# Kernel optimization log

Measured on AMD Instinct MI355X. Metric: run time of the kernel, lower is better.

## Reference

```python
import jax, jax.numpy as jnp
import numpy as np

DIM, HEADS = 1024, 16
HEAD_DIM = DIM // HEADS
SCALE = HEAD_DIM ** -0.5


def setup_inputs() -> dict:
    key = jax.random.key(0)
    ks = jax.random.split(key, 5)
    B, N = 2, 2048
    x = jax.random.normal(ks[0], (B, N, DIM), dtype=jnp.float32)
    freqs = jax.random.normal(ks[1], (N, HEAD_DIM // 2), dtype=jnp.float32)
    w_qkv = jax.random.normal(ks[2], (3 * DIM, DIM), dtype=jnp.float32) * 0.02
    w_proj = jax.random.normal(ks[3], (DIM, DIM), dtype=jnp.float32) * 0.02
    b_proj = jnp.zeros((DIM,), dtype=jnp.float32)
    return {"x": x, "freqs": freqs, "w_qkv": w_qkv, "w_proj": w_proj, "b_proj": b_proj}


def _apply_rotary(t, cos, sin):
    # t: (B,N,H,D); cos/sin: (1,N,1,D//2)
    B, N, H, D = t.shape
    tp = t.reshape(B, N, H, D // 2, 2)
    x1, x2 = tp[..., 0], tp[..., 1]
    out = jnp.stack([x1 * cos - x2 * sin, x1 * sin + x2 * cos], axis=-1)
    return out.reshape(B, N, H, D)


def reference(x, freqs, w_qkv, w_proj, b_proj):
    B, N, C = x.shape
    H, D = HEADS, HEAD_DIM
    qkv = (x @ w_qkv.T).reshape(B, N, 3, H, D)  # fused QKV projection
    q, k, v = qkv[:, :, 0], qkv[:, :, 1], qkv[:, :, 2]  # each (B,N,H,D)
    cos = jnp.cos(freqs)[None, :, None, :]  # (1,N,1,D/2)
    sin = jnp.sin(freqs)[None, :, None, :]
    q = _apply_rotary(q, cos, sin)
    k = _apply_rotary(k, cos, sin)
    # SDPA: scores (B,H,N,N)
    scores = jnp.einsum("bqhd,bkhd->bhqk", q, k) * SCALE
    attn = jax.nn.softmax(scores, axis=-1)
    out = jnp.einsum("bhqk,bkhd->bqhd", attn, v).reshape(B, N, C)
    return out @ w_proj.T + b_proj
```

## Files before the change

### kernel.cpp

```cpp
#include <hip/hip_runtime.h>
#include <hip/hip_bf16.h>
#include <stdint.h>

#define BATCH   2
#define SEQ     2048
#define CDIM    1024
#define NHEAD   16
#define HDIM    64
#define MROWS   (BATCH*SEQ)
#define QKVN    (3*CDIM)
#define QSCALE  0.18033688011112042f

typedef __hip_bfloat16 bf16;
using bf16x8 = __attribute__((ext_vector_type(8))) __bf16;
using f32x4  = __attribute__((ext_vector_type(4))) float;
using s16x4  = __attribute__((ext_vector_type(4))) short;

__device__ __forceinline__ void gld16(const void* g, void* l) {
    __builtin_amdgcn_global_load_lds(
        (__attribute__((address_space(1))) void*)(void*)(g),
        (__attribute__((address_space(3))) void*)(l),
        16, 0, 0);
}

__device__ __forceinline__ f32x4 mfma16x16x32(bf16x8 a, bf16x8 b, f32x4 c) {
    return __builtin_amdgcn_mfma_f32_16x16x32_bf16(a, b, c, 0, 0, 0);
}
__device__ __forceinline__ f32x4 mfma16x16x16(s16x4 a, s16x4 b, f32x4 c) {
    return __builtin_amdgcn_mfma_f32_16x16x16bf16_1k(a, b, c, 0, 0, 0);
}

__device__ __forceinline__ uint16_t bfbits(float v) {
    bf16 b = __float2bfloat16(v);
    return *(uint16_t*)&b;
}
__device__ __forceinline__ uint32_t pkbf(float a, float b) {
    uint32_t au = __builtin_bit_cast(uint32_t, a);
    uint32_t bu = __builtin_bit_cast(uint32_t, b);
    return ((au + 0x8000u) >> 16) | ((bu + 0x8000u) & 0xffff0000u);
}

#define NX_F4 ((size_t)MROWS*CDIM/4)
#define NQ_F4 ((size_t)QKVN*CDIM/4)
#define NP_F4 ((size_t)CDIM*CDIM/4)
#define NF_SC ((size_t)SEQ*32)

__global__ __launch_bounds__(256)
void cvt_kernel(const float* __restrict__ x, const float* __restrict__ wq,
                const float* __restrict__ wp, const float* __restrict__ freqs,
                bf16* __restrict__ xb, bf16* __restrict__ wqb,
                bf16* __restrict__ wpb, float2* __restrict__ csn) {
    size_t i4 = (size_t)blockIdx.x*256 + threadIdx.x;
    if (i4 < NX_F4 + NQ_F4 + NP_F4) {
        const float* src; bf16* dst; size_t off;
        if (i4 < NX_F4)           { src = x;  dst = xb;  off = i4; }
        else if (i4 < NX_F4+NQ_F4){ src = wq; dst = wqb; off = i4 - NX_F4; }
        else                      { src = wp; dst = wpb; off = i4 - NX_F4 - NQ_F4; }
        float4 v = ((const float4*)src)[off];
        bf16 o[4] = { __float2bfloat16(v.x), __float2bfloat16(v.y),
                      __float2bfloat16(v.z), __float2bfloat16(v.w) };
        *(uint64_t*)(dst + off*4) = *(const uint64_t*)o;
    } else if (i4 < NX_F4 + NQ_F4 + NP_F4 + NF_SC) {
        size_t k = i4 - (NX_F4 + NQ_F4 + NP_F4);
        float f = freqs[k];
        csn[k] = make_float2(cosf(f), sinf(f));
    }
}

__global__ __launch_bounds__(256)
void gemm_qkv_rope(const bf16* __restrict__ A, const bf16* __restrict__ Bw,
                   const float2* __restrict__ csn, bf16* __restrict__ Qr,
                   bf16* __restrict__ Kr, bf16* __restrict__ VG) {
    const int K = CDIM;
    __shared__ __align__(16) bf16 sh[64*136];
    bf16* As = sh;
    bf16* Bs = sh + 4096;

    const int bm = blockIdx.x, bn = blockIdx.y;
    const int tid  = threadIdx.x;
    const int lane = tid & 63;
    const int w    = tid >> 6;
    const int wm   = (w & 1) * 64;
    const int wn   = (w >> 1) * 64;
    const int quad = lane >> 4;
    const int l16  = lane & 15;

    const int c0 = tid, c1 = tid + 256;
    const size_t a_off0 = (size_t)(bm*128 + (c0 >> 2)) * K + (c0 & 3) * 8;
    const size_t a_off1 = (size_t)(bm*128 + (c1 >> 2)) * K + (c1 & 3) * 8;
    const size_t b_off0 = (size_t)(bn*128 + (c0 >> 2)) * K + (c0 & 3) * 8;
    const size_t b_off1 = (size_t)(bn*128 + (c1 >> 2)) * K + (c1 & 3) * 8;

    f32x4 acc[4][4] = {};

    for (int k0 = 0; k0 < K; k0 += 32) {
        __syncthreads();
        gld16(A + a_off0 + k0, &As[c0*8]);
        gld16(A + a_off1 + k0, &As[c1*8]);
        gld16(Bw + b_off0 + k0, &Bs[c0*8]);
        gld16(Bw + b_off1 + k0, &Bs[c1*8]);
        __syncthreads();

        bf16x8 af[4], bfv[4];
#pragma unroll
        for (int i = 0; i < 4; i++)
            af[i] = *(const bf16x8*)&As[(wm + i*16 + l16)*32 + quad*8];
#pragma unroll
        for (int i = 0; i < 4; i++)
            bfv[i] = *(const bf16x8*)&Bs[(wn + i*16 + l16)*32 + quad*8];
#pragma unroll
        for (int mi = 0; mi < 4; mi++)
#pragma unroll
            for (int ni = 0; ni < 4; ni++)
                acc[mi][ni] = mfma16x16x32(af[mi], bfv[ni], acc[mi][ni]);
    }

    const int region = bn >> 3;
    if (region < 2) {
        bf16* dst = region ? Kr : Qr;
        const float qs = region ? 1.0f : QSCALE;
        const int odd = l16 & 1;
#pragma unroll
        for (int mi = 0; mi < 4; mi++) {
#pragma unroll
            for (int ni = 0; ni < 4; ni++) {
                const int cq = (bn & 7)*128 + wn + ni*16 + l16;
                const int h = cq >> 6, d = cq & 63, fi = d >> 1;
#pragma unroll
                for (int r = 0; r < 4; r++) {
                    const int m = bm*128 + wm + mi*16 + quad*4 + r;
                    const int bb = m >> 11, n = m & 2047;
                    float own = acc[mi][ni][r];
                    float prt = __shfl_xor(own, 1);
                    float2 cs2 = csn[n*32 + fi];
                    float o = odd ? (prt*cs2.y + own*cs2.x)
                                  : (own*cs2.x - prt*cs2.y);
                    dst[((size_t)(bb*16 + h)*SEQ + n)*HDIM + d] =
                        __float2bfloat16(o * qs);
                }
            }
        }
    } else {
        const int bb = (bm*128) >> 11, n0l = (bm*128) & 2047;
        __syncthreads();
#pragma unroll
        for (int cc = 0; cc < 2; ++cc) {
            if ((w >> 1) == cc) {
#pragma unroll
                for (int mi = 0; mi < 4; mi++)
#pragma unroll
                    for (int ni = 0; ni < 4; ni++) {
                        const int d  = ni*16 + l16;
                        const int tl = wm + mi*16 + quad*4;
                        uint2 pk;
                        pk.x = (uint32_t)bfbits(acc[mi][ni][0]) |
                               ((uint32_t)bfbits(acc[mi][ni][1]) << 16);
                        pk.y = (uint32_t)bfbits(acc[mi][ni][2]) |
                               ((uint32_t)bfbits(acc[mi][ni][3]) << 16);
                        *(uint2*)&sh[d*136 + tl] = pk;
                    }
            }
            __syncthreads();
            const int h = (bn - 16)*2 + cc;
            bf16* vg = VG + (size_t)(bb*16 + h) * (SEQ*HDIM);
#pragma unroll
            for (int k = 0; k < 8; k++) {
                int s8   = tid + 256*k;
                int tile = s8 >> 10, si = s8 & 1023;
                int g  = si >> 6,  ln = si & 63;
                int j  = g >> 2,   dt = g & 3;
                int qk = ln >> 4,  ld = ln & 15;
                int tl = tile*64 + j*16 + qk*4;
                int d  = dt*16 + ld;
                *(uint2*)&vg[(size_t)((n0l >> 6) + tile)*4096 + si*4] =
                    *(const uint2*)&sh[d*136 + tl];
            }
            __syncthreads();
        }
    }
}

__global__ __launch_bounds__(256)
void gemm_proj(const bf16* __restrict__ A, const bf16* __restrict__ Bw,
               const float* __restrict__ bias, float* __restrict__ C,
               int M, int N, int K) {
    __shared__ __align__(16) bf16 As[64*32];
    __shared__ __align__(16) bf16 Bs[128*32];

    const int bm = blockIdx.x, bn = blockIdx.y;
    const int tid  = threadIdx.x;
    const int lane = tid & 63;
    const int w    = tid >> 6;
    const int wm   = (w & 1) * 32;
    const int wn   = (w >> 1) * 64;
    const int quad = lane >> 4;
    const int l16  = lane & 15;

    const int ca = tid, cb0 = tid, cb1 = tid + 256;
    const size_t a_off  = (size_t)(bm*64  + (ca  >> 2)) * K + (ca  & 3) * 8;
    const size_t b_off0 = (size_t)(bn*128 + (cb0 >> 2)) * K + (cb0 & 3) * 8;
    const size_t b_off1 = (size_t)(bn*128 + (cb1 >> 2)) * K + (cb1 & 3) * 8;

    f32x4 acc[2][4] = {};

    for (int k0 = 0; k0 < K; k0 += 32) {
        __syncthreads();
        gld16(A + a_off + k0, &As[ca*8]);
        gld16(Bw + b_off0 + k0, &Bs[cb0*8]);
        gld16(Bw + b_off1 + k0, &Bs[cb1*8]);
        __syncthreads();

        bf16x8 af[2], bfv[4];
#pragma unroll
        for (int i = 0; i < 2; i++)
            af[i] = *(const bf16x8*)&As[(wm + i*16 + l16)*32 + quad*8];
#pragma unroll
        for (int i = 0; i < 4; i++)
            bfv[i] = *(const bf16x8*)&Bs[(wn + i*16 + l16)*32 + quad*8];
#pragma unroll
        for (int mi = 0; mi < 2; mi++)
#pragma unroll
            for (int ni = 0; ni < 4; ni++)
                acc[mi][ni] = mfma16x16x32(af[mi], bfv[ni], acc[mi][ni]);
    }

#pragma unroll
    for (int mi = 0; mi < 2; mi++) {
        const int r0 = bm*64 + wm + mi*16 + quad*4;
#pragma unroll
        for (int ni = 0; ni < 4; ni++) {
            const int c = bn*128 + wn + ni*16 + l16;
            const float bv = bias[c];
#pragma unroll
            for (int r = 0; r < 4; r++)
                C[(size_t)(r0 + r)*N + c] = acc[mi][ni][r] + bv;
        }
    }
}

__global__ __launch_bounds__(64)
void attn_kernel(const bf16* __restrict__ Qr, const bf16* __restrict__ Kr,
                 const bf16* __restrict__ VG, bf16* __restrict__ Ao) {
    const int blk = blockIdx.x;
    const int bh  = blk >> 5;
    const int b   = bh >> 4, h = bh & 15;
    const int q0  = (blk & 31) * 64;
    const int lane = threadIdx.x;
    const int quad = lane >> 4, l16 = lane & 15;

    bf16x8 qf[4][2];
#pragma unroll
    for (int t = 0; t < 4; t++) {
        const int qrow = q0 + t*16 + l16;
        const bf16* qp = Qr + ((size_t)bh*SEQ + qrow)*HDIM + quad*8;
        qf[t][0] = *(const bf16x8*)(qp);
        qf[t][1] = *(const bf16x8*)(qp + 32);
    }

    const bf16* KrB = Kr + (size_t)bh*SEQ*HDIM;
    const bf16* VgB = VG + (size_t)bh*SEQ*HDIM;

    f32x4 acc[4][4] = {};
    float lsum[4] = {};

    bf16x8 kb0[4][2], kb1[4][2];

#pragma unroll
    for (int j = 0; j < 4; j++) {
        const bf16* kr = KrB + (size_t)(j*16 + l16)*HDIM + quad*8;
        kb0[j][0] = *(const bf16x8*)(kr);
        kb0[j][1] = *(const bf16x8*)(kr + 32);
    }

    auto step = [&](bf16x8 (&kc)[4][2], bf16x8 (&kn)[4][2], int it) {
        s16x4 vfr[16];
        const bf16* vt = VgB + (size_t)it*4096;
#pragma unroll
        for (int m = 0; m < 16; m++)
            vfr[m] = *(const s16x4*)&vt[(m*64 + lane)*4];

        if (it + 1 < SEQ/64) {
            const bf16* kr = KrB + (size_t)((it+1)*64 + l16)*HDIM + quad*8;
#pragma unroll
            for (int j = 0; j < 4; j++) {
                kn[j][0] = *(const bf16x8*)(kr + j*16*HDIM);
                kn[j][1] = *(const bf16x8*)(kr + j*16*HDIM + 32);
            }
        }

#pragma unroll
        for (int j = 0; j < 4; j++) {
            s16x4 pf[4];
#pragma unroll
            for (int t = 0; t < 4; t++) {
                f32x4 sv = {};
                sv = mfma16x16x32(kc[j][0], qf[t][0], sv);
                sv = mfma16x16x32(kc[j][1], qf[t][1], sv);
                float e0 = __builtin_amdgcn_exp2f(sv[0]);
                float e1 = __builtin_amdgcn_exp2f(sv[1]);
                float e2 = __builtin_amdgcn_exp2f(sv[2]);
                float e3 = __builtin_amdgcn_exp2f(sv[3]);
                lsum[t] += (e0 + e1) + (e2 + e3);
                union { uint32_t u[2]; s16x4 v; } pa;
                pa.u[0] = pkbf(e0, e1);
                pa.u[1] = pkbf(e2, e3);
                pf[t] = pa.v;
            }
#pragma unroll
            for (int dt = 0; dt < 4; dt++) {
                s16x4 vf = vfr[j*4 + dt];
#pragma unroll
                for (int t = 0; t < 4; t++)
                    acc[t][dt] = mfma16x16x16(pf[t], vf, acc[t][dt]);
            }
        }
    };

    for (int it2 = 0; it2 < SEQ/128; ++it2) {
        step(kb0, kb1, it2*2);
        step(kb1, kb0, it2*2 + 1);
    }

#pragma unroll
    for (int t = 0; t < 4; t++) {
        lsum[t] += __shfl_xor(lsum[t], 16, 64);
        lsum[t] += __shfl_xor(lsum[t], 32, 64);
    }
    float lt[4][4];
#pragma unroll
    for (int t = 0; t < 4; t++)
#pragma unroll
        for (int r = 0; r < 4; r++)
            lt[t][r] = __shfl(lsum[t], quad*20 + r, 64);

#pragma unroll
    for (int t = 0; t < 4; t++)
#pragma unroll
        for (int dt = 0; dt < 4; dt++)
#pragma unroll
            for (int r = 0; r < 4; r++) {
                int qr  = q0 + t*16 + quad*4 + r;
                int col = h*HDIM + dt*16 + l16;
                Ao[(size_t)(b*SEQ + qr)*CDIM + col] =
                    __float2bfloat16(acc[t][dt][r] / lt[t][r]);
            }
}

extern "C" void kernel_launch(void* const* d_in, const int* in_sizes, int n_in,
                              void* d_out, int out_size, void* d_ws, size_t ws_size,
                              hipStream_t stream) {
    const float* x      = (const float*)d_in[0];
    const float* freqs  = (const float*)d_in[1];
    const float* w_qkv  = (const float*)d_in[2];
    const float* w_proj = (const float*)d_in[3];
    const float* b_proj = (const float*)d_in[4];
    float* out = (float*)d_out;

    char* ws = (char*)d_ws;
    bf16*   xb    = (bf16*)ws;   ws += (size_t)MROWS * CDIM * sizeof(bf16);
    bf16*   wqkvb = (bf16*)ws;   ws += (size_t)QKVN * CDIM * sizeof(bf16);
    bf16*   wprojb= (bf16*)ws;   ws += (size_t)CDIM * CDIM * sizeof(bf16);
    float2* csn   = (float2*)ws; ws += (size_t)SEQ * 32 * sizeof(float2);
    bf16*   Qr    = (bf16*)ws;   ws += (size_t)BATCH*NHEAD*SEQ*HDIM*sizeof(bf16);
    bf16*   Kr    = (bf16*)ws;   ws += (size_t)BATCH*NHEAD*SEQ*HDIM*sizeof(bf16);
    bf16*   VG    = (bf16*)ws;   ws += (size_t)BATCH*NHEAD*SEQ*HDIM*sizeof(bf16);
    bf16*   Ao    = (bf16*)ws;

    {
        size_t nthr = NX_F4 + NQ_F4 + NP_F4 + NF_SC;
        cvt_kernel<<<dim3((nthr + 255) / 256), dim3(256), 0, stream>>>(
            x, w_qkv, w_proj, freqs, xb, wqkvb, wprojb, csn);
    }
    gemm_qkv_rope<<<dim3(MROWS/128, QKVN/128), dim3(256), 0, stream>>>(
        xb, wqkvb, csn, Qr, Kr, VG);
    attn_kernel<<<dim3(BATCH*NHEAD*(SEQ/64)), dim3(64), 0, stream>>>(
        Qr, Kr, VG, Ao);
    gemm_proj<<<dim3(MROWS/64, CDIM/128), dim3(256), 0, stream>>>(
        Ao, wprojb, b_proj, out, MROWS, CDIM, CDIM);
}
```

Before: 229.2 us.

## Stage attention K/V through double-buffered LDS and write V directly from QKV epilogue

```diff
diff --git a/kernel.cpp b/kernel.cpp
--- a/kernel.cpp
+++ b/kernel.cpp
@@ -72,9 +72,8 @@
                    const float2* __restrict__ csn, bf16* __restrict__ Qr,
                    bf16* __restrict__ Kr, bf16* __restrict__ VG) {
     const int K = CDIM;
-    __shared__ __align__(16) bf16 sh[64*136];
-    bf16* As = sh;
-    bf16* Bs = sh + 4096;
+    __shared__ __align__(16) bf16 As[128*32];
+    __shared__ __align__(16) bf16 Bs[128*32];
 
     const int bm = blockIdx.x, bn = blockIdx.y;
     const int tid  = threadIdx.x;
@@ -141,41 +140,23 @@
             }
         }
     } else {
-        const int bb = (bm*128) >> 11, n0l = (bm*128) & 2047;
-        __syncthreads();
-#pragma unroll
-        for (int cc = 0; cc < 2; ++cc) {
-            if ((w >> 1) == cc) {
-#pragma unroll
-                for (int mi = 0; mi < 4; mi++)
-#pragma unroll
-                    for (int ni = 0; ni < 4; ni++) {
-                        const int d  = ni*16 + l16;
-                        const int tl = wm + mi*16 + quad*4;
-                        uint2 pk;
-                        pk.x = (uint32_t)bfbits(acc[mi][ni][0]) |
-                               ((uint32_t)bfbits(acc[mi][ni][1]) << 16);
-                        pk.y = (uint32_t)bfbits(acc[mi][ni][2]) |
-                               ((uint32_t)bfbits(acc[mi][ni][3]) << 16);
-                        *(uint2*)&sh[d*136 + tl] = pk;
-                    }
-            }
-            __syncthreads();
-            const int h = (bn - 16)*2 + cc;
-            bf16* vg = VG + (size_t)(bb*16 + h) * (SEQ*HDIM);
-#pragma unroll
-            for (int k = 0; k < 8; k++) {
-                int s8   = tid + 256*k;
-                int tile = s8 >> 10, si = s8 & 1023;
-                int g  = si >> 6,  ln = si & 63;
-                int j  = g >> 2,   dt = g & 3;
-                int qk = ln >> 4,  ld = ln & 15;
-                int tl = tile*64 + j*16 + qk*4;
-                int d  = dt*16 + ld;
-                *(uint2*)&vg[(size_t)((n0l >> 6) + tile)*4096 + si*4] =
-                    *(const uint2*)&sh[d*136 + tl];
-            }
-            __syncthreads();
+        const int bb  = (bm*128) >> 11, n0l = (bm*128) & 2047;
+        const int h   = (bn - 16)*2 + (wn >> 6);
+        bf16* vg = VG + (size_t)(bb*16 + h) * (SEQ*HDIM);
+#pragma unroll
+        for (int mi = 0; mi < 4; mi++) {
+            const int tile = (n0l >> 6) + ((wm + mi*16) >> 6);
+            const int j    = ((wm + mi*16) >> 4) & 3;
+#pragma unroll
+            for (int ni = 0; ni < 4; ni++) {
+                uint2 pk;
+                pk.x = (uint32_t)bfbits(acc[mi][ni][0]) |
+                       ((uint32_t)bfbits(acc[mi][ni][1]) << 16);
+                pk.y = (uint32_t)bfbits(acc[mi][ni][2]) |
+                       ((uint32_t)bfbits(acc[mi][ni][3]) << 16);
+                const int slot = (j*4 + ni)*64 + quad*16 + l16;
+                *(uint2*)&vg[(size_t)tile*4096 + slot*4] = pk;
+            }
         }
     }
 }
@@ -247,6 +228,10 @@
     const int q0  = (blk & 31) * 64;
     const int lane = threadIdx.x;
     const int quad = lane >> 4, l16 = lane & 15;
+    const int swz  = l16 & 7;
+
+    __shared__ __align__(16) bf16 Ks[2][64*64];
+    __shared__ __align__(16) bf16 Vs[2][64*64];
 
     bf16x8 qf[4][2];
 #pragma unroll
@@ -259,43 +244,54 @@
 
     const bf16* KrB = Kr + (size_t)bh*SEQ*HDIM;
     const bf16* VgB = VG + (size_t)bh*SEQ*HDIM;
+    int koff[8];
+#pragma unroll
+    for (int k = 0; k < 8; k++) {
+        int c = lane + 64*k;
+        int r = c >> 3, g = (c & 7) ^ (r & 7);
+        koff[k] = r*HDIM + g*8;
+    }
 
     f32x4 acc[4][4] = {};
     float lsum[4] = {};
 
-    bf16x8 kb0[4][2], kb1[4][2];
-
-#pragma unroll
-    for (int j = 0; j < 4; j++) {
-        const bf16* kr = KrB + (size_t)(j*16 + l16)*HDIM + quad*8;
-        kb0[j][0] = *(const bf16x8*)(kr);
-        kb0[j][1] = *(const bf16x8*)(kr + 32);
-    }
-
-    auto step = [&](bf16x8 (&kc)[4][2], bf16x8 (&kn)[4][2], int it) {
+#pragma unroll
+    for (int k = 0; k < 8; k++) {
+        gld16(KrB + koff[k], &Ks[0][(lane + 64*k)*8]);
+        gld16(VgB + (lane + 64*k)*8, &Vs[0][(lane + 64*k)*8]);
+    }
+
+    for (int it = 0; it < SEQ/64; ++it) {
+        const int cur = it & 1, nxt = cur ^ 1;
+        bf16x8 kfr[4][2];
+#pragma unroll
+        for (int j = 0; j < 4; j++) {
+            const bf16* krow = &Ks[cur][(j*16 + l16)*64];
+            kfr[j][0] = *(const bf16x8*)(krow + ((quad     ^ swz) * 8));
+            kfr[j][1] = *(const bf16x8*)(krow + (((quad+4) ^ swz) * 8));
+        }
         s16x4 vfr[16];
-        const bf16* vt = VgB + (size_t)it*4096;
 #pragma unroll
         for (int m = 0; m < 16; m++)
-            vfr[m] = *(const s16x4*)&vt[(m*64 + lane)*4];
+            vfr[m] = *(const s16x4*)&Vs[cur][(m*64 + lane)*4];
 
         if (it + 1 < SEQ/64) {
-            const bf16* kr = KrB + (size_t)((it+1)*64 + l16)*HDIM + quad*8;
-#pragma unroll
-            for (int j = 0; j < 4; j++) {
-                kn[j][0] = *(const bf16x8*)(kr + j*16*HDIM);
-                kn[j][1] = *(const bf16x8*)(kr + j*16*HDIM + 32);
-            }
-        }
-
+            const size_t o = (size_t)(it + 1) * 4096;
+#pragma unroll
+            for (int k = 0; k < 8; k++) {
+                gld16(KrB + koff[k] + o, &Ks[nxt][(lane + 64*k)*8]);
+                gld16(VgB + (lane + 64*k)*8 + o, &Vs[nxt][(lane + 64*k)*8]);
+            }
+        }
+
+        s16x4 pf[4][4];
 #pragma unroll
         for (int j = 0; j < 4; j++) {
-            s16x4 pf[4];
 #pragma unroll
             for (int t = 0; t < 4; t++) {
                 f32x4 sv = {};
-                sv = mfma16x16x32(kc[j][0], qf[t][0], sv);
-                sv = mfma16x16x32(kc[j][1], qf[t][1], sv);
+                sv = mfma16x16x32(kfr[j][0], qf[t][0], sv);
+                sv = mfma16x16x32(kfr[j][1], qf[t][1], sv);
                 float e0 = __builtin_amdgcn_exp2f(sv[0]);
                 float e1 = __builtin_amdgcn_exp2f(sv[1]);
                 float e2 = __builtin_amdgcn_exp2f(sv[2]);
@@ -304,21 +300,20 @@
                 union { uint32_t u[2]; s16x4 v; } pa;
                 pa.u[0] = pkbf(e0, e1);
                 pa.u[1] = pkbf(e2, e3);
-                pf[t] = pa.v;
-            }
-#pragma unroll
-            for (int dt = 0; dt < 4; dt++) {
+                pf[t][j] = pa.v;
+            }
+        }
+
+#pragma unroll
+        for (int dt = 0; dt < 4; dt++) {
+#pragma unroll
+            for (int j = 0; j < 4; j++) {
                 s16x4 vf = vfr[j*4 + dt];
 #pragma unroll
                 for (int t = 0; t < 4; t++)
-                    acc[t][dt] = mfma16x16x16(pf[t], vf, acc[t][dt]);
-            }
-        }
-    };
-
-    for (int it2 = 0; it2 < SEQ/128; ++it2) {
-        step(kb0, kb1, it2*2);
-        step(kb1, kb0, it2*2 + 1);
+                    acc[t][dt] = mfma16x16x16(pf[t][j], vf, acc[t][dt]);
+            }
+        }
     }
 
 #pragma unroll
```

Measured after the change: 208.3 us. 9.1% less time.
